# Kernel optimization log

Hardware: AMD Instinct MI355X
Metric: run time of the kernel (lower is better)

The kernel has to match this reference:

```python
import jax, jax.numpy as jnp
import numpy as np

N_NODES = 100000
N_EDGES = 800000
N_LAYERS = 6
GATE_TYPES = 29
H = 256        # hidden dim
INTER = 256    # inter dim
EDGE_F = 3     # (src_idx, dst_idx, reversed) edge features


def setup_inputs() -> dict:
    key = jax.random.key(0)
    ks = jax.random.split(key, 16)
    gate_type = jax.random.randint(ks[0], (N_NODES,), 0, GATE_TYPES)
    src = jax.random.randint(ks[1], (N_EDGES,), 0, N_NODES)
    dst = jax.random.randint(ks[2], (N_EDGES,), 0, N_NODES)
    w = jax.random.uniform(ks[3], (N_EDGES, EDGE_F), dtype=jnp.float32)
    s = 0.05
    emb = jax.random.normal(ks[4], (GATE_TYPES, H), dtype=jnp.float32) * s
    # QConv per layer: linear1 (no bias): [INTER, H+3]; linear2: [H, H+INTER] + bias
    W1 = jax.random.normal(ks[5], (N_LAYERS, INTER, H + EDGE_F), dtype=jnp.float32) * s
    W2 = jax.random.normal(ks[6], (N_LAYERS, H, H + INTER), dtype=jnp.float32) * s
    b2 = jax.random.normal(ks[7], (N_LAYERS, H), dtype=jnp.float32) * s
    # MLP head 256->256->1
    Wh1 = jax.random.normal(ks[8], (H, H), dtype=jnp.float32) * s
    bh1 = jax.random.normal(ks[9], (H,), dtype=jnp.float32) * s
    Wh2 = jax.random.normal(ks[10], (1, H), dtype=jnp.float32) * s
    bh2 = jax.random.normal(ks[11], (1,), dtype=jnp.float32) * s
    return {"gate_type": gate_type, "src": src, "dst": dst, "w": w,
            "emb": emb, "W1": W1, "W2": W2, "b2": b2,
            "Wh1": Wh1, "bh1": bh1, "Wh2": Wh2, "bh2": bh2}


def reference(gate_type, src, dst, w, emb, W1, W2, b2, Wh1, bh1, Wh2, bh2):
    n = gate_type.shape[0]
    h = emb[gate_type]                                   # [N, H]
    deg = jax.ops.segment_sum(jnp.ones((src.shape[0],), h.dtype), dst, num_segments=n)
    inv_deg = (1.0 / jnp.maximum(deg, 1.0))[:, None]      # mean over mailbox; 0-deg nodes -> h_N = 0
    for l in range(W1.shape[0]):
        m = jnp.concatenate([h[src], w], axis=1)          # [E, H+3] gather
        tmp = jax.nn.leaky_relu(m @ W1[l].T, 0.01)        # [E, INTER]
        h_N = jax.ops.segment_sum(tmp, dst, num_segments=n) * inv_deg  # scatter-mean [N, INTER]
        h = jax.nn.relu(jnp.concatenate([h, h_N], axis=1) @ W2[l].T + b2[l])
    x = jax.nn.relu(h @ Wh1.T + bh1)                      # [N, H]
    return x @ Wh2.T + bh2                                # [N, 1]
```

## Files before the change

kernel.cpp:

```cpp
#include <hip/hip_runtime.h>

#define H 256
#define NLAYERS 6
typedef unsigned int uint32;
typedef unsigned short u16;

typedef __bf16 bf16;
typedef bf16 bf16x8 __attribute__((ext_vector_type(8)));
typedef float f32x4 __attribute__((ext_vector_type(4)));
typedef u16 u16x8 __attribute__((ext_vector_type(8)));

__device__ __forceinline__ float bf2f(u16 h) {
    return __uint_as_float(((uint32)h) << 16);
}
__device__ __forceinline__ u16 f2bf(float f) {
    uint32 u = __float_as_uint(f);
    u = u + 0x7FFFu + ((u >> 16) & 1u);
    return (u16)(u >> 16);
}

__device__ __forceinline__ void glds16(const void* src, const char* ldsdst) {
    __builtin_amdgcn_global_load_lds(
        (const __attribute__((address_space(1))) void*)src,
        (__attribute__((address_space(3))) void*)ldsdst, 16, 0, 0);
}


__global__ __launch_bounds__(256)
void count_kernel(const int* __restrict__ dst, int* __restrict__ deg, int E) {
    int e = blockIdx.x * 256 + threadIdx.x;
    if (e < E) atomicAdd(&deg[dst[e]], 1);
}

__global__ __launch_bounds__(256)
void invd_kernel(const int* __restrict__ deg, float* __restrict__ invd, int N) {
    int n = blockIdx.x * 256 + threadIdx.x;
    if (n < N) invd[n] = 1.f / fmaxf((float)deg[n], 1.f);
}

__global__ __launch_bounds__(256)
void scan1_kernel(const int* __restrict__ deg, int* __restrict__ bsum, int N) {
    __shared__ int s[256];
    int t = threadIdx.x;
    int i = blockIdx.x * 256 + t;
    s[t] = (i < N) ? deg[i] : 0;
    __syncthreads();
    for (int off = 128; off; off >>= 1) {
        if (t < off) s[t] += s[t + off];
        __syncthreads();
    }
    if (t == 0) bsum[blockIdx.x] = s[0];
}

__global__ __launch_bounds__(512)
void scan2_kernel(int* __restrict__ bsum, int nb) {
    __shared__ int s[512];
    int t = threadIdx.x;
    int v = (t < nb) ? bsum[t] : 0;
    s[t] = v;
    __syncthreads();
    for (int off = 1; off < 512; off <<= 1) {
        int x = (t >= off) ? s[t - off] : 0;
        __syncthreads();
        s[t] += x;
        __syncthreads();
    }
    if (t < nb) bsum[t] = s[t] - v;
}

__global__ __launch_bounds__(256)
void scan3_kernel(const int* __restrict__ deg, const int* __restrict__ bsum,
                  int* __restrict__ rowptr, int N, int E) {
    __shared__ int s[256];
    int t = threadIdx.x;
    int i = blockIdx.x * 256 + t;
    int v = (i < N) ? deg[i] : 0;
    s[t] = v;
    __syncthreads();
    for (int off = 1; off < 256; off <<= 1) {
        int x = (t >= off) ? s[t - off] : 0;
        __syncthreads();
        s[t] += x;
        __syncthreads();
    }
    if (i < N) rowptr[i] = s[t] - v + bsum[blockIdx.x];
    if (i == 0) rowptr[N] = E;
}

__global__ __launch_bounds__(256)
void scatter_kernel(const int* __restrict__ src, const int* __restrict__ dst,
                    const float* __restrict__ w, const int* __restrict__ rowptr,
                    int* __restrict__ cursor, int* __restrict__ srcS,
                    float* __restrict__ wS, int E) {
    int e = blockIdx.x * 256 + threadIdx.x;
    if (e >= E) return;
    int d = dst[e];
    int p = rowptr[d] + atomicAdd(&cursor[d], 1);
    srcS[p] = src[e];
    float4 wq;
    wq.x = w[(size_t)e * 3 + 0];
    wq.y = w[(size_t)e * 3 + 1];
    wq.z = w[(size_t)e * 3 + 2];
    wq.w = 0.f;
    *(float4*)&wS[(size_t)p * 4] = wq;
}


__global__ __launch_bounds__(256)
void wsplit_kernel(const float* __restrict__ W1, const float* __restrict__ W2,
                   const float* __restrict__ Wh1,
                   u16* __restrict__ W1hi, u16* __restrict__ W1lo,
                   u16* __restrict__ W2hi, u16* __restrict__ W2lo,
                   u16* __restrict__ Wh1hi, u16* __restrict__ Wh1lo)
{
    int i = blockIdx.x * 256 + threadIdx.x;
    float v; u16* ph; u16* pl; int o;
    if (i < 393216) {
        int l = i >> 16, rem = i & 65535, r = rem >> 8, k = rem & 255;
        v = W1[(size_t)l * 66304 + (size_t)r * 259 + k];
        ph = W1hi; pl = W1lo; o = i;
    } else if (i < 1179648) {
        int j = i - 393216;
        v = W2[j];
        ph = W2hi; pl = W2lo; o = j;
    } else if (i < 1245184) {
        int j = i - 1179648;
        v = Wh1[j];
        ph = Wh1hi; pl = Wh1lo; o = j;
    } else return;
    u16 hi = f2bf(v);
    ph[o] = hi;
    pl[o] = f2bf(v - bf2f(hi));
}

__global__ void extract_kernel(const float* __restrict__ W1, float* __restrict__ ccAll)
{
    int l = blockIdx.x;
    int i = threadIdx.x;
    const float* W1l = W1 + (size_t)l * 66304;
    float* cc = ccAll + (size_t)l * 768;
    #pragma unroll
    for (int j = 0; j < 3; ++j)
        cc[j * 256 + i] = W1l[(size_t)i * 259 + 256 + j];
}


__global__ __launch_bounds__(256)
void emb_split_kernel(const int* __restrict__ gt, const float* __restrict__ emb,
                      u16* __restrict__ hHi, u16* __restrict__ hLo, int N) {
    size_t idx = (size_t)blockIdx.x * 256 + threadIdx.x;
    if (idx >= (size_t)N * 256) return;
    int n = (int)(idx >> 8), c = (int)(idx & 255);
    float v = emb[(size_t)gt[n] * 256 + c];
    u16 hi = f2bf(v);
    hHi[idx] = hi;
    hLo[idx] = f2bf(v - bf2f(hi));
}


#define LDS_AHI 0
#define LDS_ALO 8192
#define LDS_WHI 16384
#define LDS_WLO 32768

template<bool MAIN>
__device__ __forceinline__ void do_compute(const char* lds, const int* aoff,
                                           const int* woff, f32x4 (&acc)[4][4]) {
    bf16x8 ah[4], al[4];
    #pragma unroll
    for (int mi = 0; mi < 4; ++mi) {
        ah[mi] = *(const bf16x8*)(lds + LDS_AHI + aoff[mi]);
        if (MAIN) al[mi] = *(const bf16x8*)(lds + LDS_ALO + aoff[mi]);
    }
    #pragma unroll
    for (int nj = 0; nj < 4; ++nj) {
        bf16x8 wh = *(const bf16x8*)(lds + LDS_WHI + woff[nj]);
        bf16x8 wl = *(const bf16x8*)(lds + LDS_WLO + woff[nj]);
        #pragma unroll
        for (int mi = 0; mi < 4; ++mi) {
            acc[mi][nj] = __builtin_amdgcn_mfma_f32_16x16x32_bf16(wh, ah[mi], acc[mi][nj], 0, 0, 0);
            acc[mi][nj] = __builtin_amdgcn_mfma_f32_16x16x32_bf16(wl, ah[mi], acc[mi][nj], 0, 0, 0);
            if (MAIN)
                acc[mi][nj] = __builtin_amdgcn_mfma_f32_16x16x32_bf16(wh, al[mi], acc[mi][nj], 0, 0, 0);
        }
    }
}

template<int KTOT, bool BIASRELU, bool WLO>
__global__ __launch_bounds__(512)
void mfma_gemm_kernel(const u16* __restrict__ Ahi_, const u16* __restrict__ Alo_,
                      const u16* __restrict__ A2_,
                      const u16* __restrict__ Whi_, const u16* __restrict__ Wlo_,
                      const float* __restrict__ bias,
                      u16* __restrict__ Chi, u16* __restrict__ Clo, int M)
{
    __shared__ __align__(128) char lds[49152];
    const int tid = threadIdx.x;
    const int wv = tid >> 6;
    const int lane = tid & 63;
    const int m0 = blockIdx.x * 128;
    const int lrow = lane & 15, koct = lane >> 4;
    const int rh = wv & 1, cg = wv >> 1;

    int aoff[4], woff[4];
    #pragma unroll
    for (int mi = 0; mi < 4; ++mi) {
        int r = rh * 64 + mi * 16 + lrow;
        aoff[mi] = r * 64 + ((koct ^ ((r >> 1) & 3)) << 4);
    }
    #pragma unroll
    for (int nj = 0; nj < 4; ++nj) {
        int r = cg * 64 + nj * 16 + lrow;
        woff[nj] = r * 64 + ((koct ^ ((r >> 1) & 3)) << 4);
    }

    const int arow = tid >> 2;
    const int achk = (tid & 3) ^ ((arow >> 1) & 3);
    const long agrow = (long)((m0 + arow < M) ? (m0 + arow) : (M - 1));
    const char* Asrc_hi = (const char*)Ahi_ + agrow * 512 + achk * 16;
    const char* Asrc_lo = (const char*)Alo_ + agrow * 512 + achk * 16;
    const char* Asrc_2  = (const char*)A2_  + agrow * 512 + achk * 16;

    int wrow0 = tid >> 2,          wchk0 = (tid & 3) ^ ((wrow0 >> 1) & 3);
    int wrow1 = (512 + tid) >> 2,  wchk1 = ((512 + tid) & 3) ^ ((wrow1 >> 1) & 3);
    const char* Wsrc_h0 = (const char*)Whi_ + (long)wrow0 * (KTOT * 2) + wchk0 * 16;
    const char* Wsrc_h1 = (const char*)Whi_ + (long)wrow1 * (KTOT * 2) + wchk1 * 16;
    const char* Wsrc_l0 = (const char*)Wlo_ + (long)wrow0 * (KTOT * 2) + wchk0 * 16;
    const char* Wsrc_l1 = (const char*)Wlo_ + (long)wrow1 * (KTOT * 2) + wchk1 * 16;

    f32x4 acc[4][4] = {};

    for (int k0 = 0; k0 < 256; k0 += 32) {
        glds16(Asrc_hi + k0 * 2, lds + LDS_AHI + wv * 1024);
        glds16(Asrc_lo + k0 * 2, lds + LDS_ALO + wv * 1024);
        glds16(Wsrc_h0 + k0 * 2, lds + LDS_WHI + wv * 1024);
        glds16(Wsrc_h1 + k0 * 2, lds + LDS_WHI + 8192 + wv * 1024);
        glds16(Wsrc_l0 + k0 * 2, lds + LDS_WLO + wv * 1024);
        glds16(Wsrc_l1 + k0 * 2, lds + LDS_WLO + 8192 + wv * 1024);
        __syncthreads();
        do_compute<true>(lds, aoff, woff, acc);
        __syncthreads();
    }
    if (KTOT > 256) {
        for (int k0 = 256; k0 < KTOT; k0 += 32) {
            glds16(Asrc_2 + (k0 - 256) * 2, lds + LDS_AHI + wv * 1024);
            glds16(Wsrc_h0 + k0 * 2, lds + LDS_WHI + wv * 1024);
            glds16(Wsrc_h1 + k0 * 2, lds + LDS_WHI + 8192 + wv * 1024);
            glds16(Wsrc_l0 + k0 * 2, lds + LDS_WLO + wv * 1024);
            glds16(Wsrc_l1 + k0 * 2, lds + LDS_WLO + 8192 + wv * 1024);
            __syncthreads();
            do_compute<false>(lds, aoff, woff, acc);
            __syncthreads();
        }
    }

    float4 bv[4];
    if (BIASRELU) {
        #pragma unroll
        for (int nj = 0; nj < 4; ++nj)
            bv[nj] = *(const float4*)&bias[cg * 64 + nj * 16 + koct * 4];
    }
    #pragma unroll
    for (int mi = 0; mi < 4; ++mi) {
        int row = m0 + rh * 64 + mi * 16 + lrow;
        if (row >= M) continue;
        #pragma unroll
        for (int nj = 0; nj < 4; ++nj) {
            f32x4 v = acc[mi][nj];
            if (BIASRELU) {
                v[0] = fmaxf(v[0] + bv[nj].x, 0.f);
                v[1] = fmaxf(v[1] + bv[nj].y, 0.f);
                v[2] = fmaxf(v[2] + bv[nj].z, 0.f);
                v[3] = fmaxf(v[3] + bv[nj].w, 0.f);
            }
            size_t o = (size_t)row * 256 + cg * 64 + nj * 16 + koct * 4;
            ushort4 ohi;
            ohi.x = f2bf(v[0]); ohi.y = f2bf(v[1]);
            ohi.z = f2bf(v[2]); ohi.w = f2bf(v[3]);
            *(ushort4*)&Chi[o] = ohi;
            if (WLO) {
                ushort4 olo;
                olo.x = f2bf(v[0] - bf2f(ohi.x));
                olo.y = f2bf(v[1] - bf2f(ohi.y));
                olo.z = f2bf(v[2] - bf2f(ohi.z));
                olo.w = f2bf(v[3] - bf2f(ohi.w));
                *(ushort4*)&Clo[o] = olo;
            }
        }
    }
}


__global__ __launch_bounds__(256)
void edge_agg_kernel(const int* __restrict__ rowptr, const int* __restrict__ srcS,
                     const float* __restrict__ wS, const u16* __restrict__ T,
                     const float* __restrict__ cc, const float* __restrict__ invd,
                     u16* __restrict__ hN, int N) {
    int n = blockIdx.x * 4 + (threadIdx.x >> 6);
    int lane = threadIdx.x & 63;
    if (n >= N) return;
    const int half = lane >> 5;
    const int c32 = lane & 31;
    const int col0 = c32 * 8;

    float c0[8], c1[8], c2[8];
    #pragma unroll
    for (int j = 0; j < 3; ++j) {
        float4 lo4 = *(const float4*)&cc[j * 256 + col0];
        float4 hi4 = *(const float4*)&cc[j * 256 + col0 + 4];
        float* cj = (j == 0) ? c0 : (j == 1) ? c1 : c2;
        cj[0] = lo4.x; cj[1] = lo4.y; cj[2] = lo4.z; cj[3] = lo4.w;
        cj[4] = hi4.x; cj[5] = hi4.y; cj[6] = hi4.z; cj[7] = hi4.w;
    }

    float acc[8] = {};
    const int e0 = rowptr[n], e1 = rowptr[n + 1];
    int e = e0 + half;
    for (; e + 6 < e1; e += 8) {
        int s0 = srcS[e], s1 = srcS[e + 2], s2 = srcS[e + 4], s3 = srcS[e + 6];
        float4 wa = *(const float4*)&wS[(size_t)e * 4];
        float4 wb = *(const float4*)&wS[(size_t)(e + 2) * 4];
        float4 wc = *(const float4*)&wS[(size_t)(e + 4) * 4];
        float4 wd = *(const float4*)&wS[(size_t)(e + 6) * 4];
        u16x8 t0 = *(const u16x8*)&T[(size_t)s0 * 256 + col0];
        u16x8 t1 = *(const u16x8*)&T[(size_t)s1 * 256 + col0];
        u16x8 t2 = *(const u16x8*)&T[(size_t)s2 * 256 + col0];
        u16x8 t3 = *(const u16x8*)&T[(size_t)s3 * 256 + col0];
        #pragma unroll
        for (int q = 0; q < 8; ++q) {
            float x0 = fmaf(wa.x, c0[q], fmaf(wa.y, c1[q], fmaf(wa.z, c2[q], bf2f(t0[q]))));
            acc[q] += (x0 > 0.f) ? x0 : 0.01f * x0;
            float x1 = fmaf(wb.x, c0[q], fmaf(wb.y, c1[q], fmaf(wb.z, c2[q], bf2f(t1[q]))));
            acc[q] += (x1 > 0.f) ? x1 : 0.01f * x1;
            float x2 = fmaf(wc.x, c0[q], fmaf(wc.y, c1[q], fmaf(wc.z, c2[q], bf2f(t2[q]))));
            acc[q] += (x2 > 0.f) ? x2 : 0.01f * x2;
            float x3 = fmaf(wd.x, c0[q], fmaf(wd.y, c1[q], fmaf(wd.z, c2[q], bf2f(t3[q]))));
            acc[q] += (x3 > 0.f) ? x3 : 0.01f * x3;
        }
    }
    for (; e < e1; e += 2) {
        int s0 = srcS[e];
        float4 wa = *(const float4*)&wS[(size_t)e * 4];
        u16x8 t0 = *(const u16x8*)&T[(size_t)s0 * 256 + col0];
        #pragma unroll
        for (int q = 0; q < 8; ++q) {
            float x = fmaf(wa.x, c0[q], fmaf(wa.y, c1[q], fmaf(wa.z, c2[q], bf2f(t0[q]))));
            acc[q] += (x > 0.f) ? x : 0.01f * x;
        }
    }
    #pragma unroll
    for (int q = 0; q < 8; ++q) acc[q] += __shfl_xor(acc[q], 32);
    if (half == 0) {
        float sc = invd[n];
        u16x8 o;
        #pragma unroll
        for (int q = 0; q < 8; ++q) o[q] = f2bf(acc[q] * sc);
        *(u16x8*)&hN[(size_t)n * 256 + col0] = o;
    }
}


__global__ __launch_bounds__(256)
void head_out_kernel(const u16* __restrict__ xhi, const u16* __restrict__ xlo,
                     const float* __restrict__ wh2,
                     const float* __restrict__ bh2, float* __restrict__ out, int N) {
    int n = blockIdx.x * 4 + (threadIdx.x >> 6);
    int lane = threadIdx.x & 63;
    if (n >= N) return;
    ushort4 hv = ((const ushort4*)(xhi + (size_t)n * H))[lane];
    ushort4 lv = ((const ushort4*)(xlo + (size_t)n * H))[lane];
    float4 wv = ((const float4*)wh2)[lane];
    float x0 = bf2f(hv.x) + bf2f(lv.x);
    float x1 = bf2f(hv.y) + bf2f(lv.y);
    float x2 = bf2f(hv.z) + bf2f(lv.z);
    float x3 = bf2f(hv.w) + bf2f(lv.w);
    float sum = x0 * wv.x + x1 * wv.y + x2 * wv.z + x3 * wv.w;
    #pragma unroll
    for (int off = 32; off; off >>= 1) sum += __shfl_xor(sum, off);
    if (lane == 0) out[n] = sum + bh2[0];
}


extern "C" void kernel_launch(void* const* d_in, const int* in_sizes, int n_in,
                              void* d_out, int out_size, void* d_ws, size_t ws_size,
                              hipStream_t stream) {
    const int*   gate_type = (const int*)d_in[0];
    const int*   src  = (const int*)d_in[1];
    const int*   dst  = (const int*)d_in[2];
    const float* w    = (const float*)d_in[3];
    const float* emb  = (const float*)d_in[4];
    const float* W1   = (const float*)d_in[5];
    const float* W2   = (const float*)d_in[6];
    const float* b2   = (const float*)d_in[7];
    const float* Wh1  = (const float*)d_in[8];
    const float* bh1  = (const float*)d_in[9];
    const float* Wh2  = (const float*)d_in[10];
    const float* bh2  = (const float*)d_in[11];
    float* out = (float*)d_out;

    const int N = in_sizes[0];
    const int E = in_sizes[1];

    char* p = (char*)d_ws;
    auto alloc = [&](size_t bytes) -> char* {
        char* r = p;
        p += (bytes + 1023) & ~(size_t)1023;
        return r;
    };
    u16*   hHi   = (u16*)  alloc((size_t)N * H * 2);
    u16*   hLo   = (u16*)  alloc((size_t)N * H * 2);
    u16*   tBuf  = (u16*)  alloc((size_t)N * H * 2);
    u16*   hNBuf = (u16*)  alloc((size_t)N * H * 2);
    int*   srcS  = (int*)  alloc((size_t)E * 4);
    float* wS    = (float*)alloc((size_t)E * 4 * 4);
    int*   rowptr= (int*)  alloc((size_t)(N + 1) * 4);
    int*   cursor= (int*)  alloc((size_t)N * 4);
    int*   bsum  = (int*)  alloc(4096);
    float* invd  = (float*)alloc((size_t)N * 4);
    float* ccAll = (float*)alloc(6u * 768 * 4);
    u16*   W1hi  = (u16*)  alloc(6u * 256 * 256 * 2);
    u16*   W1lo  = (u16*)  alloc(6u * 256 * 256 * 2);
    u16*   W2hi  = (u16*)  alloc(6u * 256 * 512 * 2);
    u16*   W2lo  = (u16*)  alloc(6u * 256 * 512 * 2);
    u16*   Wh1hi = (u16*)  alloc(256u * 256 * 2);
    u16*   Wh1lo = (u16*)  alloc(256u * 256 * 2);

    const int nb1 = (N + 255) / 256;

    hipMemsetAsync(cursor, 0, (size_t)N * 4, stream);
    count_kernel<<<(E + 255) / 256, 256, 0, stream>>>(dst, cursor, E);
    invd_kernel<<<nb1, 256, 0, stream>>>(cursor, invd, N);
    scan1_kernel<<<nb1, 256, 0, stream>>>(cursor, bsum, N);
    scan2_kernel<<<1, 512, 0, stream>>>(bsum, nb1);
    scan3_kernel<<<nb1, 256, 0, stream>>>(cursor, bsum, rowptr, N, E);
    hipMemsetAsync(cursor, 0, (size_t)N * 4, stream);
    scatter_kernel<<<(E + 255) / 256, 256, 0, stream>>>(src, dst, w, rowptr, cursor, srcS, wS, E);

    wsplit_kernel<<<4864, 256, 0, stream>>>(W1, W2, Wh1, W1hi, W1lo, W2hi, W2lo, Wh1hi, Wh1lo);
    extract_kernel<<<6, 256, 0, stream>>>(W1, ccAll);
    emb_split_kernel<<<N, 256, 0, stream>>>(gate_type, emb, hHi, hLo, N);

    const int gm = (N + 127) / 128;
    for (int l = 0; l < NLAYERS; ++l) {
        mfma_gemm_kernel<256, false, false><<<gm, 512, 0, stream>>>(
            hHi, hLo, nullptr, W1hi + (size_t)l * 65536, W1lo + (size_t)l * 65536,
            nullptr, tBuf, nullptr, N);
        edge_agg_kernel<<<(N + 3) / 4, 256, 0, stream>>>(
            rowptr, srcS, wS, tBuf, ccAll + (size_t)l * 768, invd, hNBuf, N);
        mfma_gemm_kernel<512, true, true><<<gm, 512, 0, stream>>>(
            hHi, hLo, hNBuf, W2hi + (size_t)l * 131072, W2lo + (size_t)l * 131072,
            b2 + (size_t)l * 256, hHi, hLo, N);
    }
    mfma_gemm_kernel<256, true, true><<<gm, 512, 0, stream>>>(
        hHi, hLo, nullptr, Wh1hi, Wh1lo, bh1, hHi, hLo, N);
    head_out_kernel<<<(N + 3) / 4, 256, 0, stream>>>(hHi, hLo, Wh2, bh2, out, N);
}
```

Baseline: 2.074 ms.

## Double-buffer LDS tiles in MFMA GEMM to overlap loads with compute

Converts the split-bf16 MFMA GEMM K-loop into a double-buffered pipeline. The next K tile is loaded into a second LDS buffer while the MFMAs run on the current one, with a single waitcnt plus barrier per iteration instead of two syncthreads. This hides global-to-LDS latency, but doubles LDS use to 96KB per block, which may cut occupancy for the 512-thread blocks.

```diff
diff --git a/kernel.cpp b/kernel.cpp
--- a/kernel.cpp
+++ b/kernel.cpp
@@ -162,20 +162,21 @@
 #define LDS_ALO 8192
 #define LDS_WHI 16384
 #define LDS_WLO 32768
+#define BUFSZ   49152
 
 template<bool MAIN>
-__device__ __forceinline__ void do_compute(const char* lds, const int* aoff,
+__device__ __forceinline__ void do_compute(const char* B, const int* aoff,
                                            const int* woff, f32x4 (&acc)[4][4]) {
     bf16x8 ah[4], al[4];
     #pragma unroll
     for (int mi = 0; mi < 4; ++mi) {
-        ah[mi] = *(const bf16x8*)(lds + LDS_AHI + aoff[mi]);
-        if (MAIN) al[mi] = *(const bf16x8*)(lds + LDS_ALO + aoff[mi]);
+        ah[mi] = *(const bf16x8*)(B + LDS_AHI + aoff[mi]);
+        if (MAIN) al[mi] = *(const bf16x8*)(B + LDS_ALO + aoff[mi]);
     }
     #pragma unroll
     for (int nj = 0; nj < 4; ++nj) {
-        bf16x8 wh = *(const bf16x8*)(lds + LDS_WHI + woff[nj]);
-        bf16x8 wl = *(const bf16x8*)(lds + LDS_WLO + woff[nj]);
+        bf16x8 wh = *(const bf16x8*)(B + LDS_WHI + woff[nj]);
+        bf16x8 wl = *(const bf16x8*)(B + LDS_WLO + woff[nj]);
         #pragma unroll
         for (int mi = 0; mi < 4; ++mi) {
             acc[mi][nj] = __builtin_amdgcn_mfma_f32_16x16x32_bf16(wh, ah[mi], acc[mi][nj], 0, 0, 0);
@@ -194,7 +195,7 @@
                       const float* __restrict__ bias,
                       u16* __restrict__ Chi, u16* __restrict__ Clo, int M)
 {
-    __shared__ __align__(128) char lds[49152];
+    __shared__ __align__(128) char lds[2 * BUFSZ];
     const int tid = threadIdx.x;
     const int wv = tid >> 6;
     const int lane = tid & 63;
@@ -228,30 +229,39 @@
     const char* Wsrc_l0 = (const char*)Wlo_ + (long)wrow0 * (KTOT * 2) + wchk0 * 16;
     const char* Wsrc_l1 = (const char*)Wlo_ + (long)wrow1 * (KTOT * 2) + wchk1 * 16;
 
+    auto STAGE = [&](char* B, int t) {
+        const int k0 = t * 32;
+        if (KTOT == 256 || k0 < 256) {
+            glds16(Asrc_hi + k0 * 2, B + LDS_AHI + wv * 1024);
+            glds16(Asrc_lo + k0 * 2, B + LDS_ALO + wv * 1024);
+        } else {
+            glds16(Asrc_2 + (k0 - 256) * 2, B + LDS_AHI + wv * 1024);
+        }
+        glds16(Wsrc_h0 + k0 * 2, B + LDS_WHI + wv * 1024);
+        glds16(Wsrc_h1 + k0 * 2, B + LDS_WHI + 8192 + wv * 1024);
+        glds16(Wsrc_l0 + k0 * 2, B + LDS_WLO + wv * 1024);
+        glds16(Wsrc_l1 + k0 * 2, B + LDS_WLO + 8192 + wv * 1024);
+    };
+
     f32x4 acc[4][4] = {};
 
-    for (int k0 = 0; k0 < 256; k0 += 32) {
-        glds16(Asrc_hi + k0 * 2, lds + LDS_AHI + wv * 1024);
-        glds16(Asrc_lo + k0 * 2, lds + LDS_ALO + wv * 1024);
-        glds16(Wsrc_h0 + k0 * 2, lds + LDS_WHI + wv * 1024);
-        glds16(Wsrc_h1 + k0 * 2, lds + LDS_WHI + 8192 + wv * 1024);
-        glds16(Wsrc_l0 + k0 * 2, lds + LDS_WLO + wv * 1024);
-        glds16(Wsrc_l1 + k0 * 2, lds + LDS_WLO + 8192 + wv * 1024);
-        __syncthreads();
-        do_compute<true>(lds, aoff, woff, acc);
-        __syncthreads();
-    }
-    if (KTOT > 256) {
-        for (int k0 = 256; k0 < KTOT; k0 += 32) {
-            glds16(Asrc_2 + (k0 - 256) * 2, lds + LDS_AHI + wv * 1024);
-            glds16(Wsrc_h0 + k0 * 2, lds + LDS_WHI + wv * 1024);
-            glds16(Wsrc_h1 + k0 * 2, lds + LDS_WHI + 8192 + wv * 1024);
-            glds16(Wsrc_l0 + k0 * 2, lds + LDS_WLO + wv * 1024);
-            glds16(Wsrc_l1 + k0 * 2, lds + LDS_WLO + 8192 + wv * 1024);
-            __syncthreads();
-            do_compute<false>(lds, aoff, woff, acc);
-            __syncthreads();
-        }
+    char* bcur = lds;
+    char* bnxt = lds + BUFSZ;
+
+    STAGE(bcur, 0);
+    asm volatile("s_waitcnt vmcnt(0)" ::: "memory");
+    __builtin_amdgcn_s_barrier();
+    __builtin_amdgcn_sched_barrier(0);
+
+    const int NT = KTOT / 32;
+    for (int t = 0; t < NT; ++t) {
+        if (t + 1 < NT) STAGE(bnxt, t + 1);
+        if (KTOT == 256 || t < 8) do_compute<true>(bcur, aoff, woff, acc);
+        else                      do_compute<false>(bcur, aoff, woff, acc);
+        asm volatile("s_waitcnt lgkmcnt(0) vmcnt(0)" ::: "memory");
+        __builtin_amdgcn_s_barrier();
+        __builtin_amdgcn_sched_barrier(0);
+        char* z = bcur; bcur = bnxt; bnxt = z;
     }
 
     float4 bv[4];
```

Measured after the change: 1.936 ms. 6.7% less time.
